# Kernel tuning notes

Hardware: AMD Instinct MI355X
Metric: run time of the kernel (lower is better)

The kernel has to match this reference:

```python
import jax, jax.numpy as jnp
import numpy as np

IN_CH = 64
OUT_CH = 64
SEQ_LEN = 2048
MODES = 64  # modes2 = min(modes1, seq_len//2) = 64
SCALE = 1.0 / (IN_CH * OUT_CH)


def setup_inputs() -> dict:
    key = jax.random.key(0)
    k1, k2, k3 = jax.random.split(key, 3)
    x = jax.random.normal(k1, (32, 8, IN_CH, SEQ_LEN), dtype=jnp.float32)
    # torch.rand(...) complex init scaled by 1/(in*out): real & imag in [0, scale)
    wr = SCALE * jax.random.uniform(k2, (IN_CH, OUT_CH, MODES), dtype=jnp.float32)
    wi = SCALE * jax.random.uniform(k3, (IN_CH, OUT_CH, MODES), dtype=jnp.float32)
    return {"x": x, "wr": wr, "wi": wi}


def reference(x, wr, wi):
    # x: [B, H, E, N] real; weights complex [in, out, modes]
    N = x.shape[-1]
    w = jax.lax.complex(wr, wi)
    x_ft = jnp.fft.rfft(x)                       # [B, H, E, N//2+1] complex64
    a = x_ft[..., :MODES]                        # keep only low modes
    out_low = jnp.einsum('bjix,iox->bjox', a, w)  # per-mode complex matmul
    # zero-fill remaining frequency bins (equivalent to out_ft zeros + slice set)
    pad = N // 2 + 1 - MODES
    out_ft = jnp.pad(out_low, ((0, 0), (0, 0), (0, 0), (0, pad)))
    return jnp.fft.irfft(out_ft, n=N)            # [B, H, out_ch, N] real
```

## Files before the change

kernel.cpp:

```cpp
#include <hip/hip_runtime.h>
#include <hip/hip_bf16.h>


typedef __bf16 bf16x8 __attribute__((ext_vector_type(8)));
typedef float  f32x4  __attribute__((ext_vector_type(4)));

#define SEQ 2048
#define NM2 128
#define KS  2

__device__ __forceinline__ unsigned int rnbf(float f) {
  unsigned int u = __builtin_bit_cast(unsigned int, f);
  return (u + 0x7fffu + ((u >> 16) & 1u)) >> 16;
}
__device__ __forceinline__ unsigned int pack2(float a, float b) {
  return rnbf(a) | (rnbf(b) << 16);
}
__device__ __forceinline__ float frombf(unsigned int lo16_in_place) {
  return __builtin_bit_cast(float, lo16_in_place);
}

typedef const __attribute__((address_space(1))) unsigned int gu32;
typedef __attribute__((address_space(3))) unsigned int lu32;

__global__ __launch_bounds__(256) void k_tables(unsigned short* __restrict__ t1sw,
                                                unsigned short* __restrict__ t2sw) {
  int idx = blockIdx.x * 256 + threadIdx.x;
  int k = idx >> 11;
  int n = idx & 2047;
  float rev = (float)((k * n) & 2047) * (1.0f / 2048.0f);
  float s, co;
  asm("v_sin_f32 %0, %1" : "=v"(s)  : "v"(rev));
  asm("v_cos_f32 %0, %1" : "=v"(co) : "v"(rev));
  float ck = (k == 0 ? 1.0f : 2.0f) * (1.0f / 2048.0f);
  {
    int kt = n >> 6, part = (n >> 3) & 7, e = n & 7;
    unsigned base = (unsigned)kt * 16384u + 2u * (unsigned)e;
    unsigned offc = base + (((unsigned)(k * 128 + part * 16)) ^ (((unsigned)k & 7u) << 4));
    int c2 = k + 64;
    unsigned offs = base + (((unsigned)(c2 * 128 + part * 16)) ^ (((unsigned)c2 & 7u) << 4));
    *(unsigned short*)((char*)t1sw + offc) = (unsigned short)rnbf(co);
    *(unsigned short*)((char*)t1sw + offs) = (unsigned short)rnbf(-s);
  }
  {
    int tile = n >> 7, rl = n & 127;
    unsigned rowbase = (unsigned)tile * 32768u + (unsigned)rl * 128u;
    unsigned kpart = ((((unsigned)(k >> 3)) * 16u) ^ (((unsigned)rl & 7u) << 4)) + 2u * ((unsigned)k & 7u);
    *(unsigned short*)((char*)t2sw + rowbase + kpart)          = (unsigned short)rnbf(ck * co);
    *(unsigned short*)((char*)t2sw + rowbase + 16384u + kpart) = (unsigned short)rnbf(-ck * s);
  }
}

__global__ __launch_bounds__(256) void k_gemm1(const float* __restrict__ x,
                                               const unsigned short* __restrict__ t1sw,
                                               unsigned short* __restrict__ P) {
  __shared__ int4 lds4[65536 / 16];
  char* lds = (char*)lds4;
  const int tid = threadIdx.x, wave = tid >> 6, lane = tid & 63;
  const int mtile = blockIdx.x >> 1, ks = blockIdx.x & (KS - 1);
  const int r0 = mtile * 64;
  const int kbase = ks * (SEQ / KS);
  const char* t1base = (const char*)t1sw + (size_t)(kbase >> 6) * 16384;

  const float* xsrc[4];
#pragma unroll
  for (int p = 0; p < 4; ++p) {
    const int row = p * 16 + wave * 4 + (lane >> 4);
    const int u = (lane & 15) ^ (row & 7);
    xsrc[p] = x + (size_t)(r0 + row) * SEQ + kbase + u * 4;
  }

  f32x4 acc[8] = {};

#pragma unroll
  for (int p = 0; p < 4; ++p)
    __builtin_amdgcn_global_load_lds((gu32*)(xsrc[p]),
                                     (lu32*)(lds + p * 4096 + wave * 1024), 16, 0, 0);
#pragma unroll
  for (int p = 0; p < 4; ++p)
    __builtin_amdgcn_global_load_lds((gu32*)(t1base + (p * 256 + tid) * 16),
                                     (lu32*)(lds + 32768 + (p * 256 + wave * 64) * 16), 16, 0, 0);
  asm volatile("s_waitcnt vmcnt(0)" ::: "memory");
  __builtin_amdgcn_s_barrier();

  const int a = wave * 16 + (lane & 15);
  const unsigned xra = (unsigned)(a & 7) << 4;
  const int kg = lane >> 4;

  for (int it = 0; it < 16; ++it) {
    const int cur = it & 1, nxt = cur ^ 1;
    const int xoff = cur * 16384;
    const int toff = 32768 + cur * 16384;
    if (it < 15) {
      const char* tg = t1base + (size_t)(it + 1) * 16384;
#pragma unroll
      for (int p = 0; p < 4; ++p)
        __builtin_amdgcn_global_load_lds((gu32*)(xsrc[p] + (it + 1) * 64),
                                         (lu32*)(lds + nxt * 16384 + p * 4096 + wave * 1024),
                                         16, 0, 0);
#pragma unroll
      for (int p = 0; p < 4; ++p)
        __builtin_amdgcn_global_load_lds((gu32*)(tg + (p * 256 + tid) * 16),
                                         (lu32*)(lds + 32768 + nxt * 16384 + (p * 256 + wave * 64) * 16),
                                         16, 0, 0);
    }
#pragma unroll
    for (int kss = 0; kss < 2; ++kss) {
      const unsigned byte0 = (unsigned)(a * 256 + kss * 128 + kg * 32);
      const f32x4 lo = *(const f32x4*)(lds + xoff + (byte0 ^ xra));
      const f32x4 hi = *(const f32x4*)(lds + xoff + ((byte0 + 16) ^ xra));
      unsigned c0, c1, c2, c3;
      asm("v_cvt_pk_bf16_f32 %0, %1, %2" : "=v"(c0) : "v"(lo[0]), "v"(lo[1]));
      asm("v_cvt_pk_bf16_f32 %0, %1, %2" : "=v"(c1) : "v"(lo[2]), "v"(lo[3]));
      asm("v_cvt_pk_bf16_f32 %0, %1, %2" : "=v"(c2) : "v"(hi[0]), "v"(hi[1]));
      asm("v_cvt_pk_bf16_f32 %0, %1, %2" : "=v"(c3) : "v"(hi[2]), "v"(hi[3]));
      uint4 pk; pk.x = c0; pk.y = c1; pk.z = c2; pk.w = c3;
      const bf16x8 av = __builtin_bit_cast(bf16x8, pk);
#pragma unroll
      for (int t = 0; t < 8; ++t) {
        const int col = t * 16 + (lane & 15);
        const bf16x8 bv = *(const bf16x8*)(lds + toff +
            ((col * 128 + kss * 64 + kg * 16) ^ ((unsigned)(col & 7) << 4)));
        acc[t] = __builtin_amdgcn_mfma_f32_16x16x32_bf16(bv, av, acc[t], 0, 0, 0);
      }
    }
    asm volatile("s_waitcnt vmcnt(0)" ::: "memory");
    __builtin_amdgcn_s_barrier();
  }
  unsigned short* Pout = P + (size_t)ks * (16384 * NM2);
  const int row = r0 + wave * 16 + (lane & 15);
#pragma unroll
  for (int t = 0; t < 8; ++t) {
    const int col0 = t * 16 + kg * 4;
    uint2 v; v.x = pack2(acc[t][0], acc[t][1]); v.y = pack2(acc[t][2], acc[t][3]);
    *(uint2*)(Pout + (size_t)row * NM2 + col0) = v;
  }
}

__global__ __launch_bounds__(256) void k_stage2(const unsigned short* __restrict__ P,
                                                const float* __restrict__ wr,
                                                const float* __restrict__ wi,
                                                char* __restrict__ Bxsw) {
  __shared__ float sA[4][64][64];
  const int b = blockIdx.x;
  const int bjc = b >> 2, oh = (b >> 1) & 1, kh = b & 1;
  const int k0 = kh * 32;
  const int tid = threadIdx.x;
#pragma unroll
  for (int p = 0; p < 16; ++p) {
    int fidx = tid + 256 * p;
    int row_lin = fidx >> 4, q = fidx & 15;
    int col = (q < 8) ? (k0 + q * 4) : (64 + k0 + (q - 8) * 4);
    const unsigned short* base = P + (size_t)(bjc * 256 + row_lin) * NM2 + col;
    f32x4 v = {};
#pragma unroll
    for (int s = 0; s < KS; ++s) {
      uint2 u = *(const uint2*)(base + (size_t)s * (16384 * NM2));
      v[0] += frombf(u.x << 16);
      v[1] += frombf(u.x & 0xffff0000u);
      v[2] += frombf(u.y << 16);
      v[3] += frombf(u.y & 0xffff0000u);
    }
    *(f32x4*)(&sA[row_lin >> 6][row_lin & 63][q * 4]) = v;
  }
  __syncthreads();
  const int o_l = tid >> 3, kg = tid & 7;
  const int o = oh * 32 + o_l;
  const int kb = k0 + kg * 4;
  f32x4 accr[4] = {};
  f32x4 acci[4] = {};
  for (int i = 0; i < 64; ++i) {
    f32x4 wrv = *(const f32x4*)(wr + (i * 64 + o) * 64 + kb);
    f32x4 wiv = *(const f32x4*)(wi + (i * 64 + o) * 64 + kb);
#pragma unroll
    for (int bj = 0; bj < 4; ++bj) {
      f32x4 ar = *(const f32x4*)(&sA[bj][i][kg * 4]);
      f32x4 ai = *(const f32x4*)(&sA[bj][i][32 + kg * 4]);
#pragma unroll
      for (int kk = 0; kk < 4; ++kk) {
        accr[bj][kk] += ar[kk] * wrv[kk] - ai[kk] * wiv[kk];
        acci[bj][kk] += ar[kk] * wiv[kk] + ai[kk] * wrv[kk];
      }
    }
  }
#pragma unroll
  for (int bj = 0; bj < 4; ++bj) {
    const int r = (bjc * 4 + bj) * 64 + o;
    const int tile = r >> 7, rl = r & 127;
    char* bb = Bxsw + (size_t)tile * 32768 + (size_t)rl * 128;
    const unsigned kp = ((((unsigned)kb >> 3) * 16u) ^ (((unsigned)rl & 7u) << 4)) + 2u * ((unsigned)kb & 7u);
    uint2 vr; vr.x = pack2(accr[bj][0], accr[bj][1]); vr.y = pack2(accr[bj][2], accr[bj][3]);
    uint2 vi; vi.x = pack2(acci[bj][0], acci[bj][1]); vi.y = pack2(acci[bj][2], acci[bj][3]);
    *(uint2*)(bb + kp)          = vr;
    *(uint2*)(bb + 16384 + kp)  = vi;
  }
}

__global__ __launch_bounds__(256) void k_gemm2(const char* __restrict__ Bxsw,
                                               const char* __restrict__ t2sw,
                                               float* __restrict__ out) {
  __shared__ int4 lds4[65536 / 16];
  char* lds = (char*)lds4;
  const int tid = threadIdx.x, wave = tid >> 6, lane = tid & 63;
  const int swz = (blockIdx.x & 7) * 256 + (blockIdx.x >> 3);
  const int mb = swz >> 4, nb = swz & 15;
  const int r0 = mb * 128, n0 = nb * 128;
  const char* bsrc = Bxsw + (size_t)mb * 32768;
  const char* tsrc = t2sw + (size_t)nb * 32768;
#pragma unroll
  for (int i = 0; i < 4; ++i)
    __builtin_amdgcn_global_load_lds((gu32*)(bsrc + i * 4096 + tid * 16),
                                     (lu32*)(lds + i * 4096 + wave * 1024), 16, 0, 0);
#pragma unroll
  for (int i = 0; i < 4; ++i)
    __builtin_amdgcn_global_load_lds((gu32*)(tsrc + i * 4096 + tid * 16),
                                     (lu32*)(lds + 32768 + i * 4096 + wave * 1024), 16, 0, 0);
#pragma unroll
  for (int i = 0; i < 4; ++i)
    __builtin_amdgcn_global_load_lds((gu32*)(bsrc + 16384 + i * 4096 + tid * 16),
                                     (lu32*)(lds + 16384 + i * 4096 + wave * 1024), 16, 0, 0);
#pragma unroll
  for (int i = 0; i < 4; ++i)
    __builtin_amdgcn_global_load_lds((gu32*)(tsrc + 16384 + i * 4096 + tid * 16),
                                     (lu32*)(lds + 49152 + i * 4096 + wave * 1024), 16, 0, 0);
  asm volatile("s_waitcnt vmcnt(8)" ::: "memory");
  __builtin_amdgcn_s_barrier();

  f32x4 acc[2][8] = {};
  const int rowA0 = wave * 32 + (lane & 15);
  const int rowA1 = rowA0 + 16;
  const unsigned xa0 = (unsigned)(rowA0 & 7) << 4;
  const unsigned xa1 = (unsigned)(rowA1 & 7) << 4;

#pragma unroll
  for (int half = 0; half < 2; ++half) {
    if (half == 1) {
      asm volatile("s_waitcnt vmcnt(0)" ::: "memory");
      __builtin_amdgcn_s_barrier();
    }
    const int ab = half * 16384;
    const int bb = 32768 + half * 16384;
#pragma unroll
    for (int kq = 0; kq < 2; ++kq) {
      const unsigned offh = (unsigned)(kq * 64 + (lane >> 4) * 16);
      const bf16x8 a0 = *(const bf16x8*)(lds + ab + rowA0 * 128 + (offh ^ xa0));
      const bf16x8 a1 = *(const bf16x8*)(lds + ab + rowA1 * 128 + (offh ^ xa1));
#pragma unroll
      for (int t = 0; t < 8; ++t) {
        const int rn = t * 16 + (lane & 15);
        const bf16x8 bv = *(const bf16x8*)(lds + bb + rn * 128 + (offh ^ ((unsigned)(rn & 7) << 4)));
        acc[0][t] = __builtin_amdgcn_mfma_f32_16x16x32_bf16(a0, bv, acc[0][t], 0, 0, 0);
        acc[1][t] = __builtin_amdgcn_mfma_f32_16x16x32_bf16(a1, bv, acc[1][t], 0, 0, 0);
      }
    }
  }
#pragma unroll
  for (int m = 0; m < 2; ++m) {
#pragma unroll
    for (int j = 0; j < 4; ++j) {
      const int row = r0 + wave * 32 + m * 16 + (lane >> 4) * 4 + j;
#pragma unroll
      for (int t = 0; t < 8; ++t) {
        const int col = n0 + t * 16 + (lane & 15);
        out[(size_t)row * SEQ + col] = acc[m][t][j];
      }
    }
  }
}

extern "C" void kernel_launch(void* const* d_in, const int* in_sizes, int n_in,
                              void* d_out, int out_size, void* d_ws, size_t ws_size,
                              hipStream_t stream) {
  const float* x  = (const float*)d_in[0];
  const float* wr = (const float*)d_in[1];
  const float* wi = (const float*)d_in[2];
  float* out = (float*)d_out;
  char* ws = (char*)d_ws;
  unsigned short* t1sw = (unsigned short*)(ws);
  unsigned short* t2sw = (unsigned short*)(ws + 524288);
  unsigned short* P    = (unsigned short*)(ws + 1048576);
  char*           Bxsw = (char*)(ws + 1048576 + (size_t)KS * 16384 * NM2 * 2);

  k_tables<<<dim3(512),      dim3(256), 0, stream>>>(t1sw, t2sw);
  k_gemm1 <<<dim3(256 * KS), dim3(256), 0, stream>>>(x, t1sw, P);
  k_stage2<<<dim3(256),      dim3(256), 0, stream>>>(P, wr, wi, Bxsw);
  k_gemm2 <<<dim3(2048),     dim3(256), 0, stream>>>(Bxsw, (const char*)t2sw, out);
}
```

Baseline: 90.50 us.

## Split batch in halves and overlap gemm1 of second half with gemm2 of first

The work is split into two row halves. The second half's forward GEMM and the first half's inverse GEMM now run in one merged kernel, with blocks branching on blockIdx. Stage2 and gemm2 run per half. The goal is to fill the GPU during the under-occupied gemm1 (256 blocks) and to hide the launch tails between dependent stages. In exchange it adds two launches, and the merged kernel mixes a memory-bound workload with a compute-bound one.

```diff
diff --git a/kernel.cpp b/kernel.cpp
--- a/kernel.cpp
+++ b/kernel.cpp
@@ -51,14 +51,13 @@
   }
 }
 
-__global__ __launch_bounds__(256) void k_gemm1(const float* __restrict__ x,
-                                               const unsigned short* __restrict__ t1sw,
-                                               unsigned short* __restrict__ P) {
-  __shared__ int4 lds4[65536 / 16];
-  char* lds = (char*)lds4;
-  const int tid = threadIdx.x, wave = tid >> 6, lane = tid & 63;
-  const int mtile = blockIdx.x >> 1, ks = blockIdx.x & (KS - 1);
-  const int r0 = mtile * 64;
+__device__ __forceinline__ void gemm1_body(char* lds, int bid, int rowbase,
+                                           const float* __restrict__ x,
+                                           const unsigned short* __restrict__ t1sw,
+                                           unsigned short* __restrict__ P, int tid) {
+  const int wave = tid >> 6, lane = tid & 63;
+  const int mtile = bid >> 1, ks = bid & (KS - 1);
+  const int r0 = rowbase + mtile * 64;
   const int kbase = ks * (SEQ / KS);
   const char* t1base = (const char*)t1sw + (size_t)(kbase >> 6) * 16384;
 
@@ -137,13 +136,111 @@
   }
 }
 
+__device__ __forceinline__ void gemm2_body(char* lds, int bid, int mbbase,
+                                           const char* __restrict__ Bxsw,
+                                           const char* __restrict__ t2sw,
+                                           float* __restrict__ out, int tid) {
+  const int wave = tid >> 6, lane = tid & 63;
+  const int swz = (bid & 7) * 128 + (bid >> 3);
+  const int mb = mbbase + (swz >> 4), nb = swz & 15;
+  const int r0 = mb * 128, n0 = nb * 128;
+  const char* bsrc = Bxsw + (size_t)mb * 32768;
+  const char* tsrc = t2sw + (size_t)nb * 32768;
+#pragma unroll
+  for (int i = 0; i < 4; ++i)
+    __builtin_amdgcn_global_load_lds((gu32*)(bsrc + i * 4096 + tid * 16),
+                                     (lu32*)(lds + i * 4096 + wave * 1024), 16, 0, 0);
+#pragma unroll
+  for (int i = 0; i < 4; ++i)
+    __builtin_amdgcn_global_load_lds((gu32*)(tsrc + i * 4096 + tid * 16),
+                                     (lu32*)(lds + 32768 + i * 4096 + wave * 1024), 16, 0, 0);
+#pragma unroll
+  for (int i = 0; i < 4; ++i)
+    __builtin_amdgcn_global_load_lds((gu32*)(bsrc + 16384 + i * 4096 + tid * 16),
+                                     (lu32*)(lds + 16384 + i * 4096 + wave * 1024), 16, 0, 0);
+#pragma unroll
+  for (int i = 0; i < 4; ++i)
+    __builtin_amdgcn_global_load_lds((gu32*)(tsrc + 16384 + i * 4096 + tid * 16),
+                                     (lu32*)(lds + 49152 + i * 4096 + wave * 1024), 16, 0, 0);
+  asm volatile("s_waitcnt vmcnt(8)" ::: "memory");
+  __builtin_amdgcn_s_barrier();
+
+  f32x4 acc[2][8] = {};
+  const int rowA0 = wave * 32 + (lane & 15);
+  const int rowA1 = rowA0 + 16;
+  const unsigned xa0 = (unsigned)(rowA0 & 7) << 4;
+  const unsigned xa1 = (unsigned)(rowA1 & 7) << 4;
+
+#pragma unroll
+  for (int half = 0; half < 2; ++half) {
+    if (half == 1) {
+      asm volatile("s_waitcnt vmcnt(0)" ::: "memory");
+      __builtin_amdgcn_s_barrier();
+    }
+    const int ab = half * 16384;
+    const int bb = 32768 + half * 16384;
+#pragma unroll
+    for (int kq = 0; kq < 2; ++kq) {
+      const unsigned offh = (unsigned)(kq * 64 + (lane >> 4) * 16);
+      const bf16x8 a0 = *(const bf16x8*)(lds + ab + rowA0 * 128 + (offh ^ xa0));
+      const bf16x8 a1 = *(const bf16x8*)(lds + ab + rowA1 * 128 + (offh ^ xa1));
+#pragma unroll
+      for (int t = 0; t < 8; ++t) {
+        const int rn = t * 16 + (lane & 15);
+        const bf16x8 bv = *(const bf16x8*)(lds + bb + rn * 128 + (offh ^ ((unsigned)(rn & 7) << 4)));
+        acc[0][t] = __builtin_amdgcn_mfma_f32_16x16x32_bf16(a0, bv, acc[0][t], 0, 0, 0);
+        acc[1][t] = __builtin_amdgcn_mfma_f32_16x16x32_bf16(a1, bv, acc[1][t], 0, 0, 0);
+      }
+    }
+  }
+#pragma unroll
+  for (int m = 0; m < 2; ++m) {
+#pragma unroll
+    for (int j = 0; j < 4; ++j) {
+      const int row = r0 + wave * 32 + m * 16 + (lane >> 4) * 4 + j;
+#pragma unroll
+      for (int t = 0; t < 8; ++t) {
+        const int col = n0 + t * 16 + (lane & 15);
+        out[(size_t)row * SEQ + col] = acc[m][t][j];
+      }
+    }
+  }
+}
+
+__global__ __launch_bounds__(256) void k_gemm1(const float* __restrict__ x,
+                                               const unsigned short* __restrict__ t1sw,
+                                               unsigned short* __restrict__ P) {
+  __shared__ int4 lds4[65536 / 16];
+  gemm1_body((char*)lds4, blockIdx.x, 0, x, t1sw, P, threadIdx.x);
+}
+
+__global__ __launch_bounds__(256) void k_gemm2h1(const char* __restrict__ Bxsw,
+                                                 const char* __restrict__ t2sw,
+                                                 float* __restrict__ out) {
+  __shared__ int4 lds4[65536 / 16];
+  gemm2_body((char*)lds4, blockIdx.x, 64, Bxsw, t2sw, out, threadIdx.x);
+}
+
+__global__ __launch_bounds__(256) void k_merged(const float* __restrict__ x,
+                                                const unsigned short* __restrict__ t1sw,
+                                                unsigned short* __restrict__ P,
+                                                const char* __restrict__ Bxsw,
+                                                const char* __restrict__ t2sw,
+                                                float* __restrict__ out) {
+  __shared__ int4 lds4[65536 / 16];
+  if (blockIdx.x < 256)
+    gemm1_body((char*)lds4, blockIdx.x, 8192, x, t1sw, P, threadIdx.x);
+  else
+    gemm2_body((char*)lds4, blockIdx.x - 256, 0, Bxsw, t2sw, out, threadIdx.x);
+}
+
 __global__ __launch_bounds__(256) void k_stage2(const unsigned short* __restrict__ P,
                                                 const float* __restrict__ wr,
                                                 const float* __restrict__ wi,
-                                                char* __restrict__ Bxsw) {
+                                                char* __restrict__ Bxsw, int half) {
   __shared__ float sA[4][64][64];
   const int b = blockIdx.x;
-  const int bjc = b >> 2, oh = (b >> 1) & 1, kh = b & 1;
+  const int bjc = (b >> 2) + half * 32, oh = (b >> 1) & 1, kh = b & 1;
   const int k0 = kh * 32;
   const int tid = threadIdx.x;
 #pragma unroll
@@ -193,78 +290,6 @@
     uint2 vi; vi.x = pack2(acci[bj][0], acci[bj][1]); vi.y = pack2(acci[bj][2], acci[bj][3]);
     *(uint2*)(bb + kp)          = vr;
     *(uint2*)(bb + 16384 + kp)  = vi;
-  }
-}
-
-__global__ __launch_bounds__(256) void k_gemm2(const char* __restrict__ Bxsw,
-                                               const char* __restrict__ t2sw,
-                                               float* __restrict__ out) {
-  __shared__ int4 lds4[65536 / 16];
-  char* lds = (char*)lds4;
-  const int tid = threadIdx.x, wave = tid >> 6, lane = tid & 63;
-  const int swz = (blockIdx.x & 7) * 256 + (blockIdx.x >> 3);
-  const int mb = swz >> 4, nb = swz & 15;
-  const int r0 = mb * 128, n0 = nb * 128;
-  const char* bsrc = Bxsw + (size_t)mb * 32768;
-  const char* tsrc = t2sw + (size_t)nb * 32768;
-#pragma unroll
-  for (int i = 0; i < 4; ++i)
-    __builtin_amdgcn_global_load_lds((gu32*)(bsrc + i * 4096 + tid * 16),
-                                     (lu32*)(lds + i * 4096 + wave * 1024), 16, 0, 0);
-#pragma unroll
-  for (int i = 0; i < 4; ++i)
-    __builtin_amdgcn_global_load_lds((gu32*)(tsrc + i * 4096 + tid * 16),
-                                     (lu32*)(lds + 32768 + i * 4096 + wave * 1024), 16, 0, 0);
-#pragma unroll
-  for (int i = 0; i < 4; ++i)
-    __builtin_amdgcn_global_load_lds((gu32*)(bsrc + 16384 + i * 4096 + tid * 16),
-                                     (lu32*)(lds + 16384 + i * 4096 + wave * 1024), 16, 0, 0);
-#pragma unroll
-  for (int i = 0; i < 4; ++i)
-    __builtin_amdgcn_global_load_lds((gu32*)(tsrc + 16384 + i * 4096 + tid * 16),
-                                     (lu32*)(lds + 49152 + i * 4096 + wave * 1024), 16, 0, 0);
-  asm volatile("s_waitcnt vmcnt(8)" ::: "memory");
-  __builtin_amdgcn_s_barrier();
-
-  f32x4 acc[2][8] = {};
-  const int rowA0 = wave * 32 + (lane & 15);
-  const int rowA1 = rowA0 + 16;
-  const unsigned xa0 = (unsigned)(rowA0 & 7) << 4;
-  const unsigned xa1 = (unsigned)(rowA1 & 7) << 4;
-
-#pragma unroll
-  for (int half = 0; half < 2; ++half) {
-    if (half == 1) {
-      asm volatile("s_waitcnt vmcnt(0)" ::: "memory");
-      __builtin_amdgcn_s_barrier();
-    }
-    const int ab = half * 16384;
-    const int bb = 32768 + half * 16384;
-#pragma unroll
-    for (int kq = 0; kq < 2; ++kq) {
-      const unsigned offh = (unsigned)(kq * 64 + (lane >> 4) * 16);
-      const bf16x8 a0 = *(const bf16x8*)(lds + ab + rowA0 * 128 + (offh ^ xa0));
-      const bf16x8 a1 = *(const bf16x8*)(lds + ab + rowA1 * 128 + (offh ^ xa1));
-#pragma unroll
-      for (int t = 0; t < 8; ++t) {
-        const int rn = t * 16 + (lane & 15);
-        const bf16x8 bv = *(const bf16x8*)(lds + bb + rn * 128 + (offh ^ ((unsigned)(rn & 7) << 4)));
-        acc[0][t] = __builtin_amdgcn_mfma_f32_16x16x32_bf16(a0, bv, acc[0][t], 0, 0, 0);
-        acc[1][t] = __builtin_amdgcn_mfma_f32_16x16x32_bf16(a1, bv, acc[1][t], 0, 0, 0);
-      }
-    }
-  }
-#pragma unroll
-  for (int m = 0; m < 2; ++m) {
-#pragma unroll
-    for (int j = 0; j < 4; ++j) {
-      const int row = r0 + wave * 32 + m * 16 + (lane >> 4) * 4 + j;
-#pragma unroll
-      for (int t = 0; t < 8; ++t) {
-        const int col = n0 + t * 16 + (lane & 15);
-        out[(size_t)row * SEQ + col] = acc[m][t][j];
-      }
-    }
   }
 }
 
@@ -281,8 +306,11 @@
   unsigned short* P    = (unsigned short*)(ws + 1048576);
   char*           Bxsw = (char*)(ws + 1048576 + (size_t)KS * 16384 * NM2 * 2);
 
-  k_tables<<<dim3(512),      dim3(256), 0, stream>>>(t1sw, t2sw);
-  k_gemm1 <<<dim3(256 * KS), dim3(256), 0, stream>>>(x, t1sw, P);
-  k_stage2<<<dim3(256),      dim3(256), 0, stream>>>(P, wr, wi, Bxsw);
-  k_gemm2 <<<dim3(2048),     dim3(256), 0, stream>>>(Bxsw, (const char*)t2sw, out);
-}
+  k_tables<<<dim3(512),  dim3(256), 0, stream>>>(t1sw, t2sw);
+  k_gemm1 <<<dim3(256),  dim3(256), 0, stream>>>(x, t1sw, P);
+  k_stage2<<<dim3(128),  dim3(256), 0, stream>>>(P, wr, wi, Bxsw, 0);
+  k_merged<<<dim3(1280), dim3(256), 0, stream>>>(x, t1sw, P, Bxsw,
+                                                 (const char*)t2sw, out);
+  k_stage2<<<dim3(128),  dim3(256), 0, stream>>>(P, wr, wi, Bxsw, 1);
+  k_gemm2h1<<<dim3(1024), dim3(256), 0, stream>>>(Bxsw, (const char*)t2sw, out);
+}
```

Result: slower. 123.4 us (+36.4%).
